# Performance work log

Hardware: AMD Instinct MI355X
Metric: run time of the kernel (lower is better)

Reference implementation:

```python
import jax, jax.numpy as jnp
import numpy as np

N = 50000   # nodes
E = 800000  # edges
D = 128     # embed_dim
H = 8       # num_heads
DK = D // H # d_k = 16


def _xavier(k, shape):
    lim = np.sqrt(6.0 / (shape[0] + shape[1])).astype(np.float32)
    return jax.random.uniform(k, shape, jnp.float32, -lim, lim)


def setup_inputs() -> dict:
    key = jax.random.key(0)
    ks = jax.random.split(key, 8)
    x = jax.random.normal(ks[0], (N, D), jnp.float32)
    edge_index = jax.random.randint(ks[1], (2, E), 0, N, jnp.int64)
    att_bias = jax.random.normal(ks[2], (E, H), jnp.float32)
    # Linear weights stored as [in, out] (torch stores [out, in]; math identical)
    Wq = _xavier(ks[3], (D, D)); bq = jnp.zeros((D,), jnp.float32)
    Wk = _xavier(ks[4], (D, D)); bk = jnp.zeros((D,), jnp.float32)
    Wv = _xavier(ks[5], (D, D)); bv = jnp.zeros((D,), jnp.float32)
    Wo = _xavier(ks[6], (D, D)); bo = jnp.zeros((D,), jnp.float32)
    return {"x": x, "edge_index": edge_index, "att_bias": att_bias,
            "Wq": Wq, "bq": bq, "Wk": Wk, "bk": bk,
            "Wv": Wv, "bv": bv, "Wo": Wo, "bo": bo}


def reference(x, edge_index, att_bias, Wq, bq, Wk, bk, Wv, bv, Wo, bo):
    n = x.shape[0]
    e = edge_index.shape[1]
    h = att_bias.shape[1]
    dk = Wq.shape[1] // h
    dst = edge_index[0]  # query-side node per edge (segment ids)
    src = edge_index[1]  # key/value-side node per edge

    # project on nodes (N x D GEMMs), then gather per edge -> [E, H, DK]
    q = (x @ Wq + bq)[dst].reshape(e, h, dk)
    k = (x @ Wk + bk)[src].reshape(e, h, dk)
    v = (x @ Wv + bv)[src].reshape(e, h, dk)

    scale = 1.0 / np.sqrt(dk).astype(np.float32)
    logits = scale * jnp.sum(q * k, axis=2, keepdims=True)  # [E, H, 1]
    logits = logits + att_bias[..., None]

    # segmented (scatter) softmax over edges grouped by dst node
    seg_max = jax.ops.segment_max(logits, dst, num_segments=n)   # [N, H, 1]
    ex = jnp.exp(logits - seg_max[dst])
    seg_sum = jax.ops.segment_sum(ex, dst, num_segments=n)        # [N, H, 1]
    scores = ex / seg_sum[dst]                                    # [E, H, 1]

    # weighted scatter-sum aggregation -> [N, H, DK]
    agg = jax.ops.segment_sum(scores * v, dst, num_segments=n)
    out = agg.reshape(n, h * dk) @ Wo + bo                        # [N, D]
    return out, logits
```

## Files before the change

### kernel.cpp

```cpp
#include <hip/hip_runtime.h>
#include <hip/hip_bf16.h>
#include <math.h>


typedef __bf16 bf16x8 __attribute__((ext_vector_type(8)));
typedef float  f32x4  __attribute__((ext_vector_type(4)));

__device__ __forceinline__ ushort f32_to_bf16(float f) {
    uint u = __float_as_uint(f);
    u += 0x7FFF + ((u >> 16) & 1);
    return (ushort)(u >> 16);
}
__device__ __forceinline__ uint pack_bf16x2(float a, float b) {
    return (uint)f32_to_bf16(a) | ((uint)f32_to_bf16(b) << 16);
}
__device__ __forceinline__ float bf_lo(uint w) { return __uint_as_float(w << 16); }
__device__ __forceinline__ float bf_hi(uint w) { return __uint_as_float(w & 0xFFFF0000u); }

template<int LDC, bool OUT_BF16>
__global__ __launch_bounds__(256) void gemm_mfma(
    const ushort* __restrict__ A, const ushort* __restrict__ Bt,
    const float* __restrict__ bias, void* __restrict__ Cv, int M)
{
    __shared__ uint4 As4[2048];
    __shared__ uint4 Bs4[2048];
    const int tid  = threadIdx.x;
    const int wave = tid >> 6;
    const int lane = tid & 63;
    const int qd   = lane >> 4;
    const int ln   = lane & 15;
    const int rowBase = blockIdx.x * 128;
    const int colBase = blockIdx.y * 128;

    const uint4* gA = (const uint4*)(A + (size_t)rowBase * 128);
    #pragma unroll
    for (int i = 0; i < 8; ++i) {
        int c  = tid + i * 256;
        int lc = (c & ~15) | ((c ^ (c >> 4)) & 15);
        As4[lc] = gA[c];
    }
    const uint4* gB = (const uint4*)(Bt + (size_t)colBase * 128);
    #pragma unroll
    for (int i = 0; i < 8; ++i) {
        int c  = tid + i * 256;
        int lc = (c & ~15) | ((c ^ (c >> 4)) & 15);
        Bs4[lc] = gB[c];
    }
    __syncthreads();

    f32x4 acc[2][8];
    #pragma unroll
    for (int i = 0; i < 2; ++i)
        #pragma unroll
        for (int j = 0; j < 8; ++j)
            acc[i][j] = (f32x4){0.f, 0.f, 0.f, 0.f};

    const int m0 = wave * 32;
    #pragma unroll
    for (int ks = 0; ks < 4; ++ks) {
        const int kc = ks * 4 + qd;
        bf16x8 a0 = *((const bf16x8*)&As4[(m0 +      ln) * 16 + (kc ^ ln)]);
        bf16x8 a1 = *((const bf16x8*)&As4[(m0 + 16 + ln) * 16 + (kc ^ ln)]);
        #pragma unroll
        for (int j = 0; j < 8; ++j) {
            bf16x8 b = *((const bf16x8*)&Bs4[(j * 16 + ln) * 16 + (kc ^ ln)]);
            acc[0][j] = __builtin_amdgcn_mfma_f32_16x16x32_bf16(b, a0, acc[0][j], 0, 0, 0);
            acc[1][j] = __builtin_amdgcn_mfma_f32_16x16x32_bf16(b, a1, acc[1][j], 0, 0, 0);
        }
    }

    #pragma unroll
    for (int i = 0; i < 2; ++i) {
        int gr = rowBase + m0 + i * 16 + ln;
        if (gr < M) {
            #pragma unroll
            for (int j = 0; j < 8; ++j) {
                int coln = colBase + j * 16 + qd * 4;
                float4 b4 = *((const float4*)(bias + coln));
                float v0 = acc[i][j][0] + b4.x;
                float v1 = acc[i][j][1] + b4.y;
                float v2 = acc[i][j][2] + b4.z;
                float v3 = acc[i][j][3] + b4.w;
                if (OUT_BF16) {
                    uint2 o;
                    o.x = pack_bf16x2(v0, v1);
                    o.y = pack_bf16x2(v2, v3);
                    *((uint2*)((ushort*)Cv + (size_t)gr * LDC + coln)) = o;
                } else {
                    float4 o = make_float4(v0, v1, v2, v3);
                    *((float4*)((float*)Cv + (size_t)gr * LDC + coln)) = o;
                }
            }
        }
    }
}

__global__ __launch_bounds__(256) void prep_kernel(
    const float* __restrict__ x,
    const float* __restrict__ Wq, const float* __restrict__ Wk,
    const float* __restrict__ Wv, const float* __restrict__ bq,
    const float* __restrict__ bk, const float* __restrict__ bv,
    const float* __restrict__ Wo,
    ushort* __restrict__ WcatT, float* __restrict__ bcatI, ushort* __restrict__ WoT,
    ushort* __restrict__ xb, int* __restrict__ cnt, int N, int Mpad, int GSZ)
{
    const int gid = blockIdx.x * 256 + threadIdx.x;

    for (int i = gid; i < N; i += GSZ) cnt[i] = 0;

    const int WTOT = 384 * 128 + 384 + 128 * 128;
    for (int idx = gid; idx < WTOT; idx += GSZ) {
        if (idx < 384 * 128) {
            int jj = idx >> 7, k = idx & 127;
            const float* W; int c;
            if (jj < 128)      { W = Wq; c = jj; }
            else if (jj < 256) { W = Wk; c = jj - 128; }
            else               { W = Wv; c = jj - 256; }
            WcatT[idx] = f32_to_bf16(W[k * 128 + c]);
        } else if (idx < 384 * 128 + 384) {
            int jj = idx - 384 * 128;
            float b;
            if (jj < 128)      b = bq[jj];
            else if (jj < 256) b = bk[jj - 128];
            else               b = bv[jj - 256];
            bcatI[jj] = b;
        } else {
            int t = idx - (384 * 128 + 384);
            int n = t >> 7, k = t & 127;
            WoT[t] = f32_to_bf16(Wo[k * 128 + n]);
        }
    }

    for (int i = gid; i < Mpad * 32; i += GSZ) {
        int r = i >> 5;
        ushort4 o;
        if (r < N) {
            float4 v = ((const float4*)x)[i];
            o.x = f32_to_bf16(v.x); o.y = f32_to_bf16(v.y);
            o.z = f32_to_bf16(v.z); o.w = f32_to_bf16(v.w);
        } else {
            o.x = o.y = o.z = o.w = 0;
        }
        ((ushort4*)xb)[i] = o;
    }
}

__global__ void hist_kernel(const int* __restrict__ dst, int* __restrict__ cnt,
                            int* __restrict__ rank, int E)
{
    int e = blockIdx.x * 256 + threadIdx.x;
    if (e < E) rank[e] = atomicAdd(&cnt[dst[e]], 1);
}

__global__ __launch_bounds__(256) void scan_block(const int* __restrict__ cnt,
                                                  int* __restrict__ incl,
                                                  int* __restrict__ bsum, int N)
{
    __shared__ int sd[256];
    int tid = threadIdx.x;
    int i = blockIdx.x * 256 + tid;
    int v = (i < N) ? cnt[i] : 0;
    sd[tid] = v;
    __syncthreads();
    #pragma unroll
    for (int o = 1; o < 256; o <<= 1) {
        int t = (tid >= o) ? sd[tid - o] : 0;
        __syncthreads();
        sd[tid] += t;
        __syncthreads();
    }
    if (i < N) incl[i] = sd[tid];
    if (tid == 255) bsum[blockIdx.x] = sd[255];
}

__global__ __launch_bounds__(256) void scan_finish(
    const int* __restrict__ cnt, const int* __restrict__ incl,
    const int* __restrict__ bsum, int* __restrict__ offp,
    int N, int E, int nblk)
{
    __shared__ int sd[256];
    __shared__ int pfx;
    int tid = threadIdx.x;
    int v = (tid < nblk) ? bsum[tid] : 0;
    sd[tid] = v;
    __syncthreads();
    #pragma unroll
    for (int o = 1; o < 256; o <<= 1) {
        int t = (tid >= o) ? sd[tid - o] : 0;
        __syncthreads();
        sd[tid] += t;
        __syncthreads();
    }
    if (tid == blockIdx.x) pfx = sd[tid] - v;
    __syncthreads();
    int i = blockIdx.x * 256 + tid;
    if (i < N) offp[i] = incl[i] - cnt[i] + pfx;
    if (i == 0) offp[N] = E;
}

__global__ void scatter_kernel(const int* __restrict__ dst, const int* __restrict__ srcs,
                               const int* __restrict__ rank, const int* __restrict__ offp,
                               int2* __restrict__ pairs, const float* __restrict__ att_bias,
                               float* __restrict__ biasS, int E, int useS)
{
    int e = blockIdx.x * 256 + threadIdx.x;
    if (e < E) {
        int slot = offp[dst[e]] + rank[e];
        pairs[slot] = make_int2(srcs[e], e);
        if (useS) {
            float4 b0 = ((const float4*)att_bias)[e * 2];
            float4 b1 = ((const float4*)att_bias)[e * 2 + 1];
            ((float4*)biasS)[(size_t)slot * 2]     = b0;
            ((float4*)biasS)[(size_t)slot * 2 + 1] = b1;
        }
    }
}

__global__ __launch_bounds__(256) void attn_kernel(
    const ushort* __restrict__ Cb, const int* __restrict__ off,
    const int2* __restrict__ pairs, const float* __restrict__ att_bias,
    const float* __restrict__ biasS, int useS,
    float* __restrict__ logits_out, ushort* __restrict__ aggb, int N)
{
    const int wv   = threadIdx.x >> 6;
    const int lane = threadIdx.x & 63;
    const int node = blockIdx.x * 4 + wv;
    if (node >= N) return;
    const int eg   = lane >> 4;
    const int r    = lane & 15;
    const int h    = r >> 1;
    const int half = lane & 1;

    const char* cb = (const char*)Cb;

    uint4 qw = *((const uint4*)(cb + (size_t)node * 768) + r);
    const float q0 = bf_lo(qw.x), q1 = bf_hi(qw.x);
    const float q2 = bf_lo(qw.y), q3 = bf_hi(qw.y);
    const float q4 = bf_lo(qw.z), q5 = bf_hi(qw.z);
    const float q6 = bf_lo(qw.w), q7 = bf_hi(qw.w);

    const int s = off[node];
    const int e = off[node + 1];

    float l = 0.f;
    float a0 = 0.f, a1 = 0.f, a2 = 0.f, a3 = 0.f;
    float a4 = 0.f, a5 = 0.f, a6 = 0.f, a7 = 0.f;

    for (int b0 = s; b0 < e; b0 += 64) {
        const int cnt = min(64, e - b0);
        int gidx = b0 + ((lane < cnt) ? lane : (cnt - 1));
        int2 se = pairs[gidx];
        int regSrc = se.x;
        int regEid = se.y;

        for (int g = 0; g < cnt; g += 4) {
            int  idxr  = g + eg;
            bool valid = idxr < cnt;
            int  idxc  = valid ? idxr : (cnt - 1);
            int  srcn  = __shfl(regSrc, idxc);
            int  eid   = __shfl(regEid, idxc);
            const char* kv = cb + (size_t)((uint)srcn * 768u);
            uint4 kw = *((const uint4*)(kv + 256) + r);
            uint4 vw = *((const uint4*)(kv + 512) + r);
            float bb = useS ? biasS[(uint)(b0 + idxc) * 8u + h]
                            : att_bias[eid * 8 + h];

            float p = q0 * bf_lo(kw.x) + q1 * bf_hi(kw.x)
                    + q2 * bf_lo(kw.y) + q3 * bf_hi(kw.y)
                    + q4 * bf_lo(kw.z) + q5 * bf_hi(kw.z)
                    + q6 * bf_lo(kw.w) + q7 * bf_hi(kw.w);
            p += __shfl_xor(p, 1);
            float logit = p * 0.25f + bb;
            if (valid && half == 0) logits_out[eid * 8 + h] = logit;
            float pe = valid ? __expf(logit) : 0.f;
            l += pe;
            a0 = fmaf(pe, bf_lo(vw.x), a0); a1 = fmaf(pe, bf_hi(vw.x), a1);
            a2 = fmaf(pe, bf_lo(vw.y), a2); a3 = fmaf(pe, bf_hi(vw.y), a3);
            a4 = fmaf(pe, bf_lo(vw.z), a4); a5 = fmaf(pe, bf_hi(vw.z), a5);
            a6 = fmaf(pe, bf_lo(vw.w), a6); a7 = fmaf(pe, bf_hi(vw.w), a7);
        }
    }

    #pragma unroll
    for (int m = 16; m <= 32; m <<= 1) {
        l  += __shfl_xor(l, m);
        a0 += __shfl_xor(a0, m); a1 += __shfl_xor(a1, m);
        a2 += __shfl_xor(a2, m); a3 += __shfl_xor(a3, m);
        a4 += __shfl_xor(a4, m); a5 += __shfl_xor(a5, m);
        a6 += __shfl_xor(a6, m); a7 += __shfl_xor(a7, m);
    }
    float inv = (l > 0.f) ? (1.f / l) : 0.f;
    if (eg == 0) {
        uint4 o;
        o.x = pack_bf16x2(a0 * inv, a1 * inv);
        o.y = pack_bf16x2(a2 * inv, a3 * inv);
        o.z = pack_bf16x2(a4 * inv, a5 * inv);
        o.w = pack_bf16x2(a6 * inv, a7 * inv);
        ((uint4*)(aggb + (size_t)node * 128))[r] = o;
    }
}

extern "C" void kernel_launch(void* const* d_in, const int* in_sizes, int n_in,
                              void* d_out, int out_size, void* d_ws, size_t ws_size,
                              hipStream_t stream)
{
    const float* x        = (const float*)d_in[0];
    const int*   ei       = (const int*)d_in[1];
    const float* att_bias = (const float*)d_in[2];
    const float* Wq = (const float*)d_in[3];  const float* bq = (const float*)d_in[4];
    const float* Wk = (const float*)d_in[5];  const float* bk = (const float*)d_in[6];
    const float* Wv = (const float*)d_in[7];  const float* bv = (const float*)d_in[8];
    const float* Wo = (const float*)d_in[9];  const float* bo = (const float*)d_in[10];

    const int N = in_sizes[0] / 128;
    const int E = in_sizes[1] / 2;

    float* out    = (float*)d_out;
    float* logits = out + (size_t)N * 128;

    char* ws = (char*)d_ws;
    size_t o = 0;
    auto alloc = [&](size_t bytes) -> char* {
        char* p = ws + o;
        o = (o + bytes + 255) & ~(size_t)255;
        return p;
    };
    const int Mpad = ((N + 127) / 128) * 128;
    ushort* Cb    = (ushort*)alloc((size_t)N * 384 * 2);
    ushort* aggb  = (ushort*)alloc((size_t)Mpad * 128 * 2);
    ushort* xb    = (ushort*)alloc((size_t)Mpad * 128 * 2);
    ushort* WcatT = (ushort*)alloc((size_t)384 * 128 * 2);
    float*  bcatI = (float*)alloc(384 * 4);
    ushort* WoT   = (ushort*)alloc((size_t)128 * 128 * 2);
    int*    cnt   = (int*)alloc((size_t)N * 4);
    int*    incl  = (int*)alloc((size_t)N * 4);
    int*    rank  = (int*)alloc((size_t)E * 4);
    const int NBLK = (N + 255) / 256;
    int*    bsum  = (int*)alloc((size_t)NBLK * 4);
    int*    offp  = (int*)alloc((size_t)(N + 1) * 4);
    int2*   pairs = (int2*)alloc((size_t)E * 8);
    float*  biasS = (float*)alloc((size_t)E * 8 * 4);
    const int useS = (o <= ws_size) ? 1 : 0;
    if (!useS) biasS = nullptr;

    const int MB  = (N + 127) / 128;
    const int nbE = (E + 255) / 256;

    const int PREP_BLOCKS = 1024;
    prep_kernel<<<PREP_BLOCKS, 256, 0, stream>>>(
        x, Wq, Wk, Wv, bq, bk, bv, Wo, WcatT, bcatI, WoT, xb, cnt,
        N, Mpad, PREP_BLOCKS * 256);

    dim3 g1(MB, 3);
    gemm_mfma<384, true><<<g1, 256, 0, stream>>>(xb, WcatT, bcatI, Cb, N);

    hist_kernel<<<nbE, 256, 0, stream>>>(ei, cnt, rank, E);
    scan_block<<<NBLK, 256, 0, stream>>>(cnt, incl, bsum, N);
    scan_finish<<<NBLK, 256, 0, stream>>>(cnt, incl, bsum, offp, N, E, NBLK);
    scatter_kernel<<<nbE, 256, 0, stream>>>(ei, ei + E, rank, offp, pairs,
                                            att_bias, biasS, E, useS);

    attn_kernel<<<(N + 3) / 4, 256, 0, stream>>>(Cb, offp, pairs, att_bias,
                                                 biasS, useS, logits, aggb, N);

    dim3 g2(MB, 1);
    gemm_mfma<128, false><<<g2, 256, 0, stream>>>(aggb, WoT, bo, out, N);
}
```

Baseline: 296.3 us.

## Fuse x bf16 conversion and edge histogram into QKV GEMM, drop sorted bias copy

The QKV GEMM now reads fp32 x directly and converts it to bf16 while staging to LDS, so the separate bf16 copy of x disappears. Each block loops over the three output column tiles to reuse the A tile, and the edge histogram atomics are appended to the GEMM kernel's tail. The scatter kernel no longer copies att_bias into dst-sorted order, and the attention kernel instead reads att_bias with random access by edge id. This removes a kernel launch and several full-array passes, at the cost of a GEMM grid one third the size and uncoalesced bias gathers.

After: 270.4 us. -8.7%, faster.

```diff
diff --git a/kernel.cpp b/kernel.cpp
--- a/kernel.cpp
+++ b/kernel.cpp
@@ -17,10 +17,12 @@
 __device__ __forceinline__ float bf_lo(uint w) { return __uint_as_float(w << 16); }
 __device__ __forceinline__ float bf_hi(uint w) { return __uint_as_float(w & 0xFFFF0000u); }
 
-template<int LDC, bool OUT_BF16>
+template<int LDC, bool OUT_BF16, bool A_FP32, int NT>
 __global__ __launch_bounds__(256) void gemm_mfma(
-    const ushort* __restrict__ A, const ushort* __restrict__ Bt,
-    const float* __restrict__ bias, void* __restrict__ Cv, int M)
+    const void* __restrict__ Av, const ushort* __restrict__ Bt,
+    const float* __restrict__ bias, void* __restrict__ Cv, int M,
+    const int* __restrict__ histDst, int* __restrict__ histCnt,
+    int* __restrict__ histRank, int histE)
 {
     __shared__ uint4 As4[2048];
     __shared__ uint4 Bs4[2048];
@@ -30,79 +32,106 @@
     const int qd   = lane >> 4;
     const int ln   = lane & 15;
     const int rowBase = blockIdx.x * 128;
-    const int colBase = blockIdx.y * 128;
-
-    const uint4* gA = (const uint4*)(A + (size_t)rowBase * 128);
+
+    if (A_FP32) {
+        const float4* gA = (const float4*)((const float*)Av + (size_t)rowBase * 128);
+        #pragma unroll
+        for (int i = 0; i < 16; ++i) {
+            int c32 = tid + i * 256;
+            int r   = c32 >> 5;
+            float4 v = make_float4(0.f, 0.f, 0.f, 0.f);
+            if (rowBase + r < M) v = gA[c32];
+            ushort4 hh;
+            hh.x = f32_to_bf16(v.x); hh.y = f32_to_bf16(v.y);
+            hh.z = f32_to_bf16(v.z); hh.w = f32_to_bf16(v.w);
+            int c16 = c32 >> 1;
+            int lc  = (c16 & ~15) | ((c16 ^ (c16 >> 4)) & 15);
+            ((ushort4*)As4)[lc * 2 + (c32 & 1)] = hh;
+        }
+    } else {
+        const uint4* gA = (const uint4*)((const ushort*)Av + (size_t)rowBase * 128);
+        #pragma unroll
+        for (int i = 0; i < 8; ++i) {
+            int c  = tid + i * 256;
+            int lc = (c & ~15) | ((c ^ (c >> 4)) & 15);
+            As4[lc] = gA[c];
+        }
+    }
+
     #pragma unroll
-    for (int i = 0; i < 8; ++i) {
-        int c  = tid + i * 256;
-        int lc = (c & ~15) | ((c ^ (c >> 4)) & 15);
-        As4[lc] = gA[c];
-    }
-    const uint4* gB = (const uint4*)(Bt + (size_t)colBase * 128);
-    #pragma unroll
-    for (int i = 0; i < 8; ++i) {
-        int c  = tid + i * 256;
-        int lc = (c & ~15) | ((c ^ (c >> 4)) & 15);
-        Bs4[lc] = gB[c];
-    }
-    __syncthreads();
-
-    f32x4 acc[2][8];
-    #pragma unroll
-    for (int i = 0; i < 2; ++i)
-        #pragma unroll
-        for (int j = 0; j < 8; ++j)
-            acc[i][j] = (f32x4){0.f, 0.f, 0.f, 0.f};
-
-    const int m0 = wave * 32;
-    #pragma unroll
-    for (int ks = 0; ks < 4; ++ks) {
-        const int kc = ks * 4 + qd;
-        bf16x8 a0 = *((const bf16x8*)&As4[(m0 +      ln) * 16 + (kc ^ ln)]);
-        bf16x8 a1 = *((const bf16x8*)&As4[(m0 + 16 + ln) * 16 + (kc ^ ln)]);
-        #pragma unroll
-        for (int j = 0; j < 8; ++j) {
-            bf16x8 b = *((const bf16x8*)&Bs4[(j * 16 + ln) * 16 + (kc ^ ln)]);
-            acc[0][j] = __builtin_amdgcn_mfma_f32_16x16x32_bf16(b, a0, acc[0][j], 0, 0, 0);
-            acc[1][j] = __builtin_amdgcn_mfma_f32_16x16x32_bf16(b, a1, acc[1][j], 0, 0, 0);
-        }
-    }
-
-    #pragma unroll
-    for (int i = 0; i < 2; ++i) {
-        int gr = rowBase + m0 + i * 16 + ln;
-        if (gr < M) {
+    for (int by = 0; by < NT; ++by) {
+        const int colBase = by * 128;
+        if (by > 0) __syncthreads();
+        const uint4* gB = (const uint4*)(Bt + (size_t)colBase * 128);
+        #pragma unroll
+        for (int i = 0; i < 8; ++i) {
+            int c  = tid + i * 256;
+            int lc = (c & ~15) | ((c ^ (c >> 4)) & 15);
+            Bs4[lc] = gB[c];
+        }
+        __syncthreads();
+
+        f32x4 acc[2][8];
+        #pragma unroll
+        for (int i = 0; i < 2; ++i)
+            #pragma unroll
+            for (int j = 0; j < 8; ++j)
+                acc[i][j] = (f32x4){0.f, 0.f, 0.f, 0.f};
+
+        const int m0 = wave * 32;
+        #pragma unroll
+        for (int ks = 0; ks < 4; ++ks) {
+            const int kc = ks * 4 + qd;
+            bf16x8 a0 = *((const bf16x8*)&As4[(m0 +      ln) * 16 + (kc ^ ln)]);
+            bf16x8 a1 = *((const bf16x8*)&As4[(m0 + 16 + ln) * 16 + (kc ^ ln)]);
             #pragma unroll
             for (int j = 0; j < 8; ++j) {
-                int coln = colBase + j * 16 + qd * 4;
-                float4 b4 = *((const float4*)(bias + coln));
-                float v0 = acc[i][j][0] + b4.x;
-                float v1 = acc[i][j][1] + b4.y;
-                float v2 = acc[i][j][2] + b4.z;
-                float v3 = acc[i][j][3] + b4.w;
-                if (OUT_BF16) {
-                    uint2 o;
-                    o.x = pack_bf16x2(v0, v1);
-                    o.y = pack_bf16x2(v2, v3);
-                    *((uint2*)((ushort*)Cv + (size_t)gr * LDC + coln)) = o;
-                } else {
-                    float4 o = make_float4(v0, v1, v2, v3);
-                    *((float4*)((float*)Cv + (size_t)gr * LDC + coln)) = o;
+                bf16x8 b = *((const bf16x8*)&Bs4[(j * 16 + ln) * 16 + (kc ^ ln)]);
+                acc[0][j] = __builtin_amdgcn_mfma_f32_16x16x32_bf16(b, a0, acc[0][j], 0, 0, 0);
+                acc[1][j] = __builtin_amdgcn_mfma_f32_16x16x32_bf16(b, a1, acc[1][j], 0, 0, 0);
+            }
+        }
+
+        #pragma unroll
+        for (int i = 0; i < 2; ++i) {
+            int gr = rowBase + m0 + i * 16 + ln;
+            if (gr < M) {
+                #pragma unroll
+                for (int j = 0; j < 8; ++j) {
+                    int coln = colBase + j * 16 + qd * 4;
+                    float4 b4 = *((const float4*)(bias + coln));
+                    float v0 = acc[i][j][0] + b4.x;
+                    float v1 = acc[i][j][1] + b4.y;
+                    float v2 = acc[i][j][2] + b4.z;
+                    float v3 = acc[i][j][3] + b4.w;
+                    if (OUT_BF16) {
+                        uint2 o;
+                        o.x = pack_bf16x2(v0, v1);
+                        o.y = pack_bf16x2(v2, v3);
+                        *((uint2*)((ushort*)Cv + (size_t)gr * LDC + coln)) = o;
+                    } else {
+                        float4 o = make_float4(v0, v1, v2, v3);
+                        *((float4*)((float*)Cv + (size_t)gr * LDC + coln)) = o;
+                    }
                 }
             }
         }
     }
+
+    if (histE > 0) {
+        const int gsz = gridDim.x * 256;
+        for (int e = blockIdx.x * 256 + tid; e < histE; e += gsz)
+            histRank[e] = atomicAdd(&histCnt[histDst[e]], 1);
+    }
 }
 
 __global__ __launch_bounds__(256) void prep_kernel(
-    const float* __restrict__ x,
     const float* __restrict__ Wq, const float* __restrict__ Wk,
     const float* __restrict__ Wv, const float* __restrict__ bq,
     const float* __restrict__ bk, const float* __restrict__ bv,
     const float* __restrict__ Wo,
     ushort* __restrict__ WcatT, float* __restrict__ bcatI, ushort* __restrict__ WoT,
-    ushort* __restrict__ xb, int* __restrict__ cnt, int N, int Mpad, int GSZ)
+    int* __restrict__ cnt, int N, int GSZ)
 {
     const int gid = blockIdx.x * 256 + threadIdx.x;
 
@@ -130,26 +159,6 @@
             WoT[t] = f32_to_bf16(Wo[k * 128 + n]);
         }
     }
-
-    for (int i = gid; i < Mpad * 32; i += GSZ) {
-        int r = i >> 5;
-        ushort4 o;
-        if (r < N) {
-            float4 v = ((const float4*)x)[i];
-            o.x = f32_to_bf16(v.x); o.y = f32_to_bf16(v.y);
-            o.z = f32_to_bf16(v.z); o.w = f32_to_bf16(v.w);
-        } else {
-            o.x = o.y = o.z = o.w = 0;
-        }
-        ((ushort4*)xb)[i] = o;
-    }
-}
-
-__global__ void hist_kernel(const int* __restrict__ dst, int* __restrict__ cnt,
-                            int* __restrict__ rank, int E)
-{
-    int e = blockIdx.x * 256 + threadIdx.x;
-    if (e < E) rank[e] = atomicAdd(&cnt[dst[e]], 1);
 }
 
 __global__ __launch_bounds__(256) void scan_block(const int* __restrict__ cnt,
@@ -200,26 +209,15 @@
 
 __global__ void scatter_kernel(const int* __restrict__ dst, const int* __restrict__ srcs,
                                const int* __restrict__ rank, const int* __restrict__ offp,
-                               int2* __restrict__ pairs, const float* __restrict__ att_bias,
-                               float* __restrict__ biasS, int E, int useS)
+                               int2* __restrict__ pairs, int E)
 {
     int e = blockIdx.x * 256 + threadIdx.x;
-    if (e < E) {
-        int slot = offp[dst[e]] + rank[e];
-        pairs[slot] = make_int2(srcs[e], e);
-        if (useS) {
-            float4 b0 = ((const float4*)att_bias)[e * 2];
-            float4 b1 = ((const float4*)att_bias)[e * 2 + 1];
-            ((float4*)biasS)[(size_t)slot * 2]     = b0;
-            ((float4*)biasS)[(size_t)slot * 2 + 1] = b1;
-        }
-    }
+    if (e < E) pairs[offp[dst[e]] + rank[e]] = make_int2(srcs[e], e);
 }
 
 __global__ __launch_bounds__(256) void attn_kernel(
     const ushort* __restrict__ Cb, const int* __restrict__ off,
     const int2* __restrict__ pairs, const float* __restrict__ att_bias,
-    const float* __restrict__ biasS, int useS,
     float* __restrict__ logits_out, ushort* __restrict__ aggb, int N)
 {
     const int wv   = threadIdx.x >> 6;
@@ -262,8 +260,7 @@
             const char* kv = cb + (size_t)((uint)srcn * 768u);
             uint4 kw = *((const uint4*)(kv + 256) + r);
             uint4 vw = *((const uint4*)(kv + 512) + r);
-            float bb = useS ? biasS[(uint)(b0 + idxc) * 8u + h]
-                            : att_bias[eid * 8 + h];
+            float bb = att_bias[eid * 8 + h];
 
             float p = q0 * bf_lo(kw.x) + q1 * bf_hi(kw.x)
                     + q2 * bf_lo(kw.y) + q3 * bf_hi(kw.y)
@@ -328,7 +325,6 @@
     const int Mpad = ((N + 127) / 128) * 128;
     ushort* Cb    = (ushort*)alloc((size_t)N * 384 * 2);
     ushort* aggb  = (ushort*)alloc((size_t)Mpad * 128 * 2);
-    ushort* xb    = (ushort*)alloc((size_t)Mpad * 128 * 2);
     ushort* WcatT = (ushort*)alloc((size_t)384 * 128 * 2);
     float*  bcatI = (float*)alloc(384 * 4);
     ushort* WoT   = (ushort*)alloc((size_t)128 * 128 * 2);
@@ -339,30 +335,25 @@
     int*    bsum  = (int*)alloc((size_t)NBLK * 4);
     int*    offp  = (int*)alloc((size_t)(N + 1) * 4);
     int2*   pairs = (int2*)alloc((size_t)E * 8);
-    float*  biasS = (float*)alloc((size_t)E * 8 * 4);
-    const int useS = (o <= ws_size) ? 1 : 0;
-    if (!useS) biasS = nullptr;
 
     const int MB  = (N + 127) / 128;
     const int nbE = (E + 255) / 256;
 
-    const int PREP_BLOCKS = 1024;
+    const int PREP_BLOCKS = 512;
     prep_kernel<<<PREP_BLOCKS, 256, 0, stream>>>(
-        x, Wq, Wk, Wv, bq, bk, bv, Wo, WcatT, bcatI, WoT, xb, cnt,
-        N, Mpad, PREP_BLOCKS * 256);
-
-    dim3 g1(MB, 3);
-    gemm_mfma<384, true><<<g1, 256, 0, stream>>>(xb, WcatT, bcatI, Cb, N);
-
-    hist_kernel<<<nbE, 256, 0, stream>>>(ei, cnt, rank, E);
+        Wq, Wk, Wv, bq, bk, bv, Wo, WcatT, bcatI, WoT, cnt,
+        N, PREP_BLOCKS * 256);
+
+    gemm_mfma<384, true, true, 3><<<MB, 256, 0, stream>>>(
+        x, WcatT, bcatI, Cb, N, ei, cnt, rank, E);
+
     scan_block<<<NBLK, 256, 0, stream>>>(cnt, incl, bsum, N);
     scan_finish<<<NBLK, 256, 0, stream>>>(cnt, incl, bsum, offp, N, E, NBLK);
-    scatter_kernel<<<nbE, 256, 0, stream>>>(ei, ei + E, rank, offp, pairs,
-                                            att_bias, biasS, E, useS);
+    scatter_kernel<<<nbE, 256, 0, stream>>>(ei, ei + E, rank, offp, pairs, E);
 
     attn_kernel<<<(N + 3) / 4, 256, 0, stream>>>(Cb, offp, pairs, att_bias,
-                                                 biasS, useS, logits, aggb, N);
-
-    dim3 g2(MB, 1);
-    gemm_mfma<128, false><<<g2, 256, 0, stream>>>(aggb, WoT, bo, out, N);
-}
+                                                 logits, aggb, N);
+
+    gemm_mfma<128, false, false, 1><<<MB, 256, 0, stream>>>(
+        aggb, WoT, bo, out, N, nullptr, nullptr, nullptr, 0);
+}
```
